# Optimization experiments

Measured on AMD Instinct MI355X. Metric: run time of the kernel, lower is better.

Reference implementation:

```python
import jax, jax.numpy as jnp
import numpy as np
from jax import lax

S = 16  # encoder stride (patchify-conv stand-in for the CNN backbone, stride-16 feature grid)


def _conv(x, w, b, stride, padding):
    y = lax.conv_general_dilated(x, w, (stride, stride), padding,
                                 dimension_numbers=('NCHW', 'OIHW', 'NCHW'))
    return y + b[None, :, None, None]


def _l2norm(x, eps=1e-12):  # F.normalize(p=2, dim=1)
    n = jnp.sqrt(jnp.sum(x * x, axis=1, keepdims=True))
    return x / jnp.maximum(n, eps)


def _encode(frame, ew, eb, kw, kb, vw, vb, mask=None):
    feat = jax.nn.relu(_conv(frame, ew, eb, S, 'VALID'))  # [B,512,h,w]
    key = _conv(feat, kw, kb, 1, 'SAME')                  # [B,64,h,w]
    val = _conv(feat, vw, vb, 1, 'SAME')                  # [B,ed,h,w]
    if mask is not None:
        m = mask[:, None, ::S, ::S]  # torch F.interpolate 'nearest' with exact integer factor
        key = key * m
        val = val * m
    return _l2norm(key), val, feat


def _forward(query_frame, prev_frame, prev_mask, first_frame, first_mask,
             enc_q_w, enc_q_b, enc_m_w, enc_m_b,
             key_w, key_b, val_w, val_b,
             dec1_w, dec1_b, dec2_w, dec2_b, cls_w, cls_b):
    # memory bank reset + push(first), push(prev)
    k1, v1, _ = _encode(first_frame, enc_m_w, enc_m_b, key_w, key_b, val_w, val_b, first_mask)
    kp, vp, _ = _encode(prev_frame, enc_m_w, enc_m_b, key_w, key_b, val_w, val_b, prev_mask)
    qk, qv, _ = _encode(query_frame, enc_q_w, enc_q_b, key_w, key_b, val_w, val_b)
    B, Ck, h, w = qk.shape
    ed = qv.shape[1]
    mem_key = jnp.concatenate([k1.reshape(B, Ck, -1), kp.reshape(B, Ck, -1)], axis=2)  # [B,64,M]
    mem_val = jnp.concatenate([v1.reshape(B, ed, -1), vp.reshape(B, ed, -1)], axis=2)  # [B,ed,M]
    q_key = qk.reshape(B, Ck, -1)                                                      # [B,64,Q]
    # STM memory read: affinity -> softmax -> weighted sum over memory pixels
    affinity = jnp.einsum('bcq,bcm->bqm', q_key, mem_key) / jnp.sqrt(jnp.float32(Ck))
    affinity = jax.nn.softmax(affinity, axis=-1)
    mem_read = jnp.einsum('bqm,bcm->bcq', affinity, mem_val).reshape(B, ed, h, w)
    fused = jnp.concatenate([qv, mem_read], axis=1)  # [B,2*ed,h,w] (aspp=False)
    d = jax.nn.relu(_conv(fused, dec1_w, dec1_b, 1, 'SAME'))
    dec_feat = jax.nn.relu(_conv(d, dec2_w, dec2_b, 1, 'SAME'))
    logits = _conv(dec_feat, cls_w, cls_b, 1, 'SAME')
    H, W = query_frame.shape[-2], query_frame.shape[-1]
    logits_full = jax.image.resize(logits, (B, logits.shape[1], H, W), method='bilinear')  # align_corners=False
    rep_feat = _l2norm(dec_feat)
    return rep_feat, logits_full


def setup_inputs():
    key = jax.random.key(0)
    ks = jax.random.split(key, 16)
    B, H, W = 8, 512, 512
    Ce, Ck, ed = 512, 64, 256
    g = lambda i, sh, s: jax.random.normal(ks[i], sh, dtype=jnp.float32) * s
    return {
        'query_frame': g(0, (B, 3, H, W), 1.0),
        'prev_frame': g(1, (B, 3, H, W), 1.0),
        'prev_mask': jnp.round(jax.random.uniform(ks[2], (B, H, W), dtype=jnp.float32)),
        'first_frame': g(3, (B, 3, H, W), 1.0),
        'first_mask': jnp.round(jax.random.uniform(ks[4], (B, H, W), dtype=jnp.float32)),
        'enc_q_w': g(5, (Ce, 3, S, S), 0.02), 'enc_q_b': jnp.zeros((Ce,), jnp.float32),
        'enc_m_w': g(6, (Ce, 3, S, S), 0.02), 'enc_m_b': jnp.zeros((Ce,), jnp.float32),
        'key_w': g(7, (Ck, Ce, 1, 1), 0.05), 'key_b': jnp.zeros((Ck,), jnp.float32),
        'val_w': g(8, (ed, Ce, 1, 1), 0.05), 'val_b': jnp.zeros((ed,), jnp.float32),
        'dec1_w': g(9, (ed, 2 * ed, 3, 3), 0.02), 'dec1_b': jnp.zeros((ed,), jnp.float32),
        'dec2_w': g(10, (ed, ed, 3, 3), 0.02), 'dec2_b': jnp.zeros((ed,), jnp.float32),
        'cls_w': g(11, (2, ed, 1, 1), 0.05), 'cls_b': jnp.zeros((2,), jnp.float32),
    }


def reference(query_frame, prev_frame, prev_mask, first_frame, first_mask,
              enc_q_w, enc_q_b, enc_m_w, enc_m_b,
              key_w, key_b, val_w, val_b,
              dec1_w, dec1_b, dec2_w, dec2_b, cls_w, cls_b):
    return _forward(query_frame, prev_frame, prev_mask, first_frame, first_mask,
                    enc_q_w, enc_q_b, enc_m_w, enc_m_b,
                    key_w, key_b, val_w, val_b,
                    dec1_w, dec1_b, dec2_w, dec2_b, cls_w, cls_b)
```

## Files before the change

### kernel.cpp

```cpp
#include <hip/hip_runtime.h>
#include <hip/hip_bf16.h>
#include <cstdint>

#define DEV __device__ __forceinline__
typedef __attribute__((ext_vector_type(8))) short short8;
typedef __attribute__((ext_vector_type(4))) float f32x4;
typedef unsigned short u16;

DEV float b2f(u16 u) { union { unsigned int i; float f; } x; x.i = (unsigned)u << 16; return x.f; }
DEV u16 f2b(float f) { __hip_bfloat16 h = __float2bfloat16(f); return *(u16*)&h; }
DEV float rdin(const void* p, size_t i, int isbf) {
  return isbf ? __bfloat162float(((const __hip_bfloat16*)p)[i]) : ((const float*)p)[i];
}
DEV void wrout(void* p, size_t i, float v, int isbf) {
  if (isbf) ((__hip_bfloat16*)p)[i] = __float2bfloat16(v);
  else      ((float*)p)[i] = v;
}
DEV short8 ld8(const void* p, size_t idx, int isbf) {
  if (isbf) return *(const short8*)((const u16*)p + idx);
  const float* f = (const float*)p + idx;
  float4 x = *(const float4*)f, y = *(const float4*)(f + 4);
  short8 r;
  r[0] = f2b(x.x); r[1] = f2b(x.y); r[2] = f2b(x.z); r[3] = f2b(x.w);
  r[4] = f2b(y.x); r[5] = f2b(y.y); r[6] = f2b(y.z); r[7] = f2b(y.w);
  return r;
}
DEV void gl16(const u16* g, u16* l) {
  __builtin_amdgcn_global_load_lds(
      (const __attribute__((address_space(1))) void*)g,
      (__attribute__((address_space(3))) void*)l, 16, 0, 0);
}
DEV void bar() {
  asm volatile("" ::: "memory");
  __builtin_amdgcn_s_barrier();
  asm volatile("" ::: "memory");
}

__global__ __launch_bounds__(256) void detect_k(const u16* w, int* flag) {
  __shared__ int cnt[256];
  int tid = threadIdx.x, c = 0;
  for (int i = tid; i < 4096; i += 256) {
    u16 v = w[i];
    int e = (v >> 7) & 0xFF;
    if (v == 0 || (e >= 0x60 && e <= 0x9F)) c++;
  }
  cnt[tid] = c;
  __syncthreads();
  for (int s = 128; s > 0; s >>= 1) { if (tid < s) cnt[tid] += cnt[tid + s]; __syncthreads(); }
  if (tid == 0) *flag = (cnt[0] > 3600) ? 1 : 0;
}

__global__ __launch_bounds__(256) void patchify_k(const void* F0, const void* F1,
                                                  u16* dst, const int* dflag) {
  int isbf = *dflag;
  int bid = blockIdx.x;
  int z = bid >> 8, rem = bid & 255, b = rem >> 5, y = rem & 31;
  const void* F = z ? F1 : F0;
  int x = threadIdx.x & 31, pj = threadIdx.x >> 5;
  u16* drow = dst + (size_t)(z * 8192 + b * 1024 + y * 32 + x) * 768;
#pragma unroll
  for (int i = 0; i < 6; i++) {
    int pair = i * 8 + pj;
    int c = pair >> 4, ky = pair & 15;
    size_t src = ((size_t)((b * 3 + c) * 512 + y * 16 + ky)) * 512 + x * 16;
    short8 v0 = ld8(F, src, isbf);
    short8 v1 = ld8(F, src + 8, isbf);
    u16* dp = drow + c * 256 + ky * 16;
    *(short8*)dp = v0;
    *(short8*)(dp + 8) = v1;
  }
}

__global__ __launch_bounds__(256) void wconv_k(const void* wm, const void* wq,
                                               u16* dst, const int* dflag) {
  int isbf = *dflag;
  int gi = blockIdx.x * 256 + threadIdx.x;
  size_t e0 = (size_t)gi * 8;
  const void* src = e0 < 393216 ? wm : wq;
  size_t off = e0 < 393216 ? e0 : e0 - 393216;
  *(short8*)&dst[e0] = ld8(src, off, isbf);
}

__global__ __launch_bounds__(256) void kvconv_k(const void* valW, const void* keyW,
                                                u16* dst, const int* dflag) {
  int isbf = *dflag;
  int idx = blockIdx.x * 256 + threadIdx.x;
  size_t e0 = (size_t)idx * 8;
  int row = (int)(e0 >> 9);
  const void* src = row < 256 ? valW : keyW;
  size_t off = row < 256 ? e0 : e0 - (size_t)256 * 512;
  *(short8*)&dst[e0] = ld8(src, off, isbf);
}

struct PA {
  const void* W0; const void* W1; size_t bs; int K; int rowsplit; int zsel; int ws16; int rowmax1;
  DEV short8 l8(int row, int k, int b, int zz, int isbf) const {
    const void* W = W0; int r = row;
    if (zsel && zz == 2) W = W1;
    else if (rowsplit && row >= rowsplit) { W = W1; r = row - rowsplit; if (r > rowmax1) r = rowmax1; }
    return ld8(W, (size_t)b * bs + (size_t)r * K + k, ws16 ? 1 : isbf);
  }
  DEV const u16* ga(int row, int k, int b, int zz) const {
    int r = row; if (rowsplit && r > rowmax1) r = rowmax1;
    return (const u16*)W0 + (size_t)b * bs + (size_t)r * K + k;
  }
};
struct PBws {
  const u16* X; int rs; size_t zs;
  DEV short8 l8(int t, int k, int zz, int) const {
    return *(const short8*)(X + (size_t)zz * zs + (size_t)t * rs + k);
  }
  DEV const u16* ga(int t, int k, int zz) const {
    return X + (size_t)zz * zs + (size_t)t * rs + k;
  }
};
struct PBc3 {
  const u16* X; int C; int shift;
  DEV short8 l8(int t, int k, int, int) const {
    int tap = k >> shift, c0 = k & (C - 1);
    int dy = tap / 3, dx = tap - dy * 3;
    int pos = t & 1023, y = pos >> 5, x = pos & 31;
    int iy = y + dy - 1, ix = x + dx - 1;
    if ((unsigned)iy >= 32u || (unsigned)ix >= 32u) { short8 z = {0,0,0,0,0,0,0,0}; return z; }
    return *(const short8*)(X + (size_t)(((t >> 10) * 1024) + iy * 32 + ix) * C + c0);
  }
};

struct Epi {
  int mode;
  u16 *o16, *o16b, *o16c;
  size_t zs; int ts, moff, mmax;
  const void *bias, *bias2; int bzsel;
  const void *maskA, *maskB;
  const float* rscale;
  float scale; int relu, doexp;
  DEV void store1(int m, int t, int z, float v, int isbf) const {
    if (m >= mmax) return;
    int b = t >> 10, pos = t & 1023;
    if (m < 256) {
      v += rdin(bias, m, isbf);
      if (z < 2) {
        const void* mk = z ? maskB : maskA;
        v *= rdin(mk, ((size_t)(b * 512 + (pos >> 5) * 16) << 9) + (pos & 31) * 16, isbf);
        o16[((size_t)(b * 256 + m)) * 2048 + (size_t)z * 1024 + pos] = f2b(v);
      } else {
        o16b[(size_t)t * 512 + m] = f2b(v);
      }
    } else {
      v += rdin(bias2, m - 256, isbf);
      o16c[((size_t)z * 8192 + t) * 64 + (m - 256)] = f2b(v);
    }
  }
};

DEV void epilogue(const Epi& ep, f32x4 (&acc)[4][4], u16* sh, int isbf, int tid,
                  int col16, int quad, int wm, int wn, int zz, int m0, int n0, int nbase) {
  if (ep.mode == 1) {
#pragma unroll
    for (int mt = 0; mt < 4; mt++)
#pragma unroll
      for (int nt = 0; nt < 4; nt++)
#pragma unroll
        for (int r = 0; r < 4; r++) {
          int m = m0 + wm * 64 + mt * 16 + quad * 4 + r;
          int t = nbase + n0 + wn * 64 + nt * 16 + col16;
          ep.store1(m, t, zz, acc[mt][nt][r], isbf);
        }
    return;
  }
  if (ep.mode == 2) {
    float* pf = (float*)ep.o16;
#pragma unroll
    for (int mt = 0; mt < 4; mt++)
#pragma unroll
      for (int nt = 0; nt < 4; nt++)
#pragma unroll
        for (int r = 0; r < 4; r++) {
          int m = m0 + wm * 64 + mt * 16 + quad * 4 + r;
          int t = nbase + n0 + wn * 64 + nt * 16 + col16;
          pf[((size_t)(zz * 256 + m)) * 8192 + t] = acc[mt][nt][r];
        }
    return;
  }
  u16* T = sh;
  const int TS = 132;
  for (int p = 0; p < 2; p++) {
    __syncthreads();
    if (wn == p) {
#pragma unroll
      for (int mt = 0; mt < 4; mt++)
#pragma unroll
        for (int nt = 0; nt < 4; nt++) {
          int tl = nt * 16 + col16;
#pragma unroll
          for (int r2 = 0; r2 < 2; r2++) {
            int ml = wm * 64 + mt * 16 + quad * 4 + r2 * 2;
            float v0 = acc[mt][nt][r2 * 2] * ep.scale;
            float v1 = acc[mt][nt][r2 * 2 + 1] * ep.scale;
            if (ep.bias) {
              const void* bp = (ep.bzsel && zz == 2) ? ep.bias2 : ep.bias;
              v0 += rdin(bp, m0 + ml, isbf);
              v1 += rdin(bp, m0 + ml + 1, isbf);
            }
            if (ep.relu) { v0 = fmaxf(v0, 0.f); v1 = fmaxf(v1, 0.f); }
            unsigned int pk = (unsigned)f2b(v0) | ((unsigned)f2b(v1) << 16);
            *(unsigned int*)&T[tl * TS + ml] = pk;
          }
        }
    }
    __syncthreads();
    {
      int tl = tid >> 2, seg = tid & 3;
      int tg = nbase + n0 + p * 64 + tl;
      u16* op = ep.o16 + (size_t)zz * ep.zs + (size_t)tg * ep.ts + ep.moff + m0;
#pragma unroll
      for (int i = 0; i < 4; i++) {
        int c8 = seg + i * 4;
        short8 v = *(short8*)&T[tl * TS + c8 * 8];
        *(short8*)&op[c8 * 8] = v;
      }
    }
  }
}

template <class PB>
__global__ __launch_bounds__(256) void mgl(PA pa, PB pb, Epi ep, int ktiles, int nbase,
                                           const int* dflag) {
  __shared__ u16 sh[32768];
  int isbf = *dflag;
  int tid = threadIdx.x, lane = tid & 63;
  int col16 = lane & 15, quad = lane >> 4;
  int wv = tid >> 6, wm = wv >> 1, wn = wv & 1;
  int zz = blockIdx.z;
  int n0 = blockIdx.x * 128, m0 = blockIdx.y * 128;
  int bA = (nbase + n0) >> 10;

  f32x4 acc[4][4];
#pragma unroll
  for (int mt = 0; mt < 4; mt++)
#pragma unroll
    for (int nt = 0; nt < 4; nt++)
#pragma unroll
      for (int r = 0; r < 4; r++) acc[mt][nt][r] = 0.f;

  int rA[4], lA[4];
#pragma unroll
  for (int g = 0; g < 4; g++) {
    rA[g] = g * 32 + (tid >> 3);
    lA[g] = (tid & 7) ^ (rA[g] & 7);
  }

  auto issue = [&](int kt) {
    int kk = kt * 64;
    u16* base = sh + ((kt & 1) << 14);
#pragma unroll
    for (int g = 0; g < 4; g++) {
      gl16(pa.ga(m0 + rA[g], kk + lA[g] * 8, bA, zz), base + (size_t)(g * 256 + tid) * 8);
      gl16(pb.ga(nbase + n0 + rA[g], kk + lA[g] * 8, zz), base + 8192 + (size_t)(g * 256 + tid) * 8);
    }
  };
  issue(0);

  for (int kt = 0; kt < ktiles; kt++) {
    const u16* As = sh + ((kt & 1) << 14);
    const u16* Bs = As + 8192;
    if (kt + 1 < ktiles) {
      issue(kt + 1);
      asm volatile("s_waitcnt vmcnt(8)" ::: "memory");
    } else {
      asm volatile("s_waitcnt vmcnt(0)" ::: "memory");
    }
    bar();
#pragma unroll
    for (int s = 0; s < 2; s++) {
      short8 af[4], bf[4];
      int cs = ((s * 4 + quad) ^ (col16 & 7)) << 3;
#pragma unroll
      for (int mt = 0; mt < 4; mt++)
        af[mt] = *(const short8*)&As[(wm * 64 + mt * 16 + col16) * 64 + cs];
#pragma unroll
      for (int nt = 0; nt < 4; nt++)
        bf[nt] = *(const short8*)&Bs[(wn * 64 + nt * 16 + col16) * 64 + cs];
#pragma unroll
      for (int mt = 0; mt < 4; mt++)
#pragma unroll
        for (int nt = 0; nt < 4; nt++)
          acc[mt][nt] = __builtin_amdgcn_mfma_f32_16x16x32_bf16(af[mt], bf[nt], acc[mt][nt], 0, 0, 0);
    }
    bar();
  }

  epilogue(ep, acc, sh, isbf, tid, col16, quad, wm, wn, zz, m0, n0, nbase);
}

template <class PB>
__global__ __launch_bounds__(256) void mg(PA pa, PB pb, Epi ep, int ktiles, int nbase,
                                          int ksplit, const int* dflag) {
  __shared__ u16 sh[32768];
  int isbf = *dflag;
  int tid = threadIdx.x, lane = tid & 63;
  int col16 = lane & 15, quad = lane >> 4;
  int wv = tid >> 6, wm = wv >> 1, wn = wv & 1;
  int zz = blockIdx.z;
  int kb = ksplit * zz;
  int n0 = blockIdx.x * 128, m0 = blockIdx.y * 128;
  int bA = (nbase + n0) >> 10;

  f32x4 acc[4][4];
#pragma unroll
  for (int mt = 0; mt < 4; mt++)
#pragma unroll
    for (int nt = 0; nt < 4; nt++)
#pragma unroll
      for (int r = 0; r < 4; r++) acc[mt][nt][r] = 0.f;

  int rA[4], lA[4];
#pragma unroll
  for (int g = 0; g < 4; g++) {
    rA[g] = g * 32 + (tid >> 3);
    lA[g] = (tid & 7) ^ (rA[g] & 7);
  }

  short8 ra[4], rb[4];
#pragma unroll
  for (int g = 0; g < 4; g++) {
    ra[g] = pa.l8(m0 + rA[g], kb + lA[g] * 8, bA, zz, isbf);
    rb[g] = pb.l8(nbase + n0 + rA[g], kb + lA[g] * 8, zz, isbf);
  }
#pragma unroll
  for (int g = 0; g < 4; g++) {
    *(short8*)&sh[(size_t)(g * 256 + tid) * 8] = ra[g];
    *(short8*)&sh[8192 + (size_t)(g * 256 + tid) * 8] = rb[g];
  }
  __syncthreads();

  for (int kt = 0; kt < ktiles; kt++) {
    const u16* As = sh + ((kt & 1) ? 16384 : 0);
    const u16* Bs = As + 8192;
    bool more = (kt + 1 < ktiles);
    if (more) {
      int kn = kb + (kt + 1) * 64;
#pragma unroll
      for (int g = 0; g < 4; g++) {
        ra[g] = pa.l8(m0 + rA[g], kn + lA[g] * 8, bA, zz, isbf);
        rb[g] = pb.l8(nbase + n0 + rA[g], kn + lA[g] * 8, zz, isbf);
      }
    }
#pragma unroll
    for (int s = 0; s < 2; s++) {
      short8 af[4], bf[4];
      int cs = ((s * 4 + quad) ^ (col16 & 7)) << 3;
#pragma unroll
      for (int mt = 0; mt < 4; mt++)
        af[mt] = *(const short8*)&As[(wm * 64 + mt * 16 + col16) * 64 + cs];
#pragma unroll
      for (int nt = 0; nt < 4; nt++)
        bf[nt] = *(const short8*)&Bs[(wn * 64 + nt * 16 + col16) * 64 + cs];
#pragma unroll
      for (int mt = 0; mt < 4; mt++)
#pragma unroll
        for (int nt = 0; nt < 4; nt++)
          acc[mt][nt] = __builtin_amdgcn_mfma_f32_16x16x32_bf16(af[mt], bf[nt], acc[mt][nt], 0, 0, 0);
    }
    if (more) {
      u16* An = sh + (!(kt & 1) ? 16384 : 0);
#pragma unroll
      for (int g = 0; g < 4; g++) {
        *(short8*)&An[(size_t)(g * 256 + tid) * 8] = ra[g];
        *(short8*)&An[8192 + (size_t)(g * 256 + tid) * 8] = rb[g];
      }
      __syncthreads();
    }
  }

  epilogue(ep, acc, sh, isbf, tid, col16, quad, wm, wn, zz, m0, n0, nbase);
}

__global__ __launch_bounds__(256) void attn_k(const u16* qk, const u16* memk,
                                              const u16* memv, float* pf, float* rsum) {
  __shared__ u16 sh[28672];
  __shared__ float rsl[4][64];
  const int Qt = 0, Kt = 4096, Vt = 8192, Pl = 24576;
  int tid = threadIdx.x, lane = tid & 63;
  int col16 = lane & 15, quad = lane >> 4;
  int wv = tid >> 6;
  int xl = blockIdx.x;
  int x = ((xl & 7) << 4) | (xl >> 3);
  int b = x >> 4, qt = x & 15;
  int q0 = b * 1024 + qt * 64;
  int s = blockIdx.y;
  int kv0 = s * 512;

  rsl[wv][lane] = 0.f;

  int r32 = tid >> 3;
#pragma unroll
  for (int g = 0; g < 2; g++) {
    int row = g * 32 + r32;
    int k8 = (tid & 7) ^ (row & 7);
    gl16(qk + (size_t)(q0 + row) * 64 + k8 * 8, sh + Qt + (size_t)(g * 256 + tid) * 8);
  }
  {
#pragma unroll
    for (int g = 0; g < 2; g++) {
      int row = g * 32 + r32;
      int k8 = (tid & 7) ^ (row & 7);
      gl16(memk + ((size_t)(b * 2048 + kv0 + row)) * 64 + k8 * 8,
           sh + Kt + (size_t)(g * 256 + tid) * 8);
    }
#pragma unroll
    for (int g = 0; g < 8; g++) {
      int row = g * 32 + r32;
      int k8 = (tid & 7) ^ (row & 7);
      gl16(memv + ((size_t)(b * 256 + row)) * 2048 + kv0 + k8 * 8,
           sh + Vt + (size_t)(g * 256 + tid) * 8);
    }
  }
  __syncthreads();

  f32x4 acc_o[4][4];
#pragma unroll
  for (int mt = 0; mt < 4; mt++)
#pragma unroll
    for (int nt = 0; nt < 4; nt++)
#pragma unroll
      for (int r = 0; r < 4; r++) acc_o[mt][nt][r] = 0.f;

  for (int ch = 0; ch < 8; ch++) {
    {
      f32x4 acc_s[4];
#pragma unroll
      for (int nt = 0; nt < 4; nt++)
#pragma unroll
        for (int r = 0; r < 4; r++) acc_s[nt][r] = 0.f;
#pragma unroll
      for (int s2 = 0; s2 < 2; s2++) {
        int cs = ((s2 * 4 + quad) ^ (col16 & 7)) << 3;
        short8 af = *(const short8*)&sh[Kt + (wv * 16 + col16) * 64 + cs];
        short8 bf[4];
#pragma unroll
        for (int nt = 0; nt < 4; nt++)
          bf[nt] = *(const short8*)&sh[Qt + (nt * 16 + col16) * 64 + cs];
#pragma unroll
        for (int nt = 0; nt < 4; nt++)
          acc_s[nt] = __builtin_amdgcn_mfma_f32_16x16x32_bf16(af, bf[nt], acc_s[nt], 0, 0, 0);
      }
#pragma unroll
      for (int nt = 0; nt < 4; nt++) {
        int ql = nt * 16 + col16;
        float tsum = 0.f;
#pragma unroll
        for (int r = 0; r < 4; r++) {
          int kvl = wv * 16 + quad * 4 + r;
          u16 pb = f2b(__expf(0.125f * acc_s[nt][r]));
          tsum += b2f(pb);
          sh[Pl + ql * 64 + (((kvl >> 3) ^ (ql & 7)) << 3) + (kvl & 7)] = pb;
        }
        tsum += __shfl_xor(tsum, 16);
        tsum += __shfl_xor(tsum, 32);
        if (quad == 0) rsl[wv][ql] += tsum;
      }
    }
    __syncthreads();
    if (ch + 1 < 8) {
      int kvc = kv0 + (ch + 1) * 64;
#pragma unroll
      for (int g = 0; g < 2; g++) {
        int row = g * 32 + r32;
        int k8 = (tid & 7) ^ (row & 7);
        gl16(memk + ((size_t)(b * 2048 + kvc + row)) * 64 + k8 * 8,
             sh + Kt + (size_t)(g * 256 + tid) * 8);
      }
    }
#pragma unroll
    for (int s2 = 0; s2 < 2; s2++) {
      short8 af[4], bf[4];
      int cs = ((s2 * 4 + quad) ^ (col16 & 7)) << 3;
#pragma unroll
      for (int mt = 0; mt < 4; mt++)
        af[mt] = *(const short8*)&sh[Vt + (wv * 64 + mt * 16 + col16) * 64 + cs];
#pragma unroll
      for (int nt = 0; nt < 4; nt++)
        bf[nt] = *(const short8*)&sh[Pl + (nt * 16 + col16) * 64 + cs];
#pragma unroll
      for (int mt = 0; mt < 4; mt++)
#pragma unroll
        for (int nt = 0; nt < 4; nt++)
          acc_o[mt][nt] = __builtin_amdgcn_mfma_f32_16x16x32_bf16(af[mt], bf[nt], acc_o[mt][nt], 0, 0, 0);
    }
    __syncthreads();
    if (ch + 1 < 8) {
      int kvc = kv0 + (ch + 1) * 64;
#pragma unroll
      for (int g = 0; g < 8; g++) {
        int row = g * 32 + r32;
        int k8 = (tid & 7) ^ (row & 7);
        gl16(memv + ((size_t)(b * 256 + row)) * 2048 + kvc + k8 * 8,
             sh + Vt + (size_t)(g * 256 + tid) * 8);
      }
    }
    __syncthreads();
  }

#pragma unroll
  for (int mt = 0; mt < 4; mt++)
#pragma unroll
    for (int nt = 0; nt < 4; nt++)
#pragma unroll
      for (int r = 0; r < 4; r++) {
        int c = wv * 64 + mt * 16 + quad * 4 + r;
        int q = nt * 16 + col16;
        pf[((size_t)(s * 8192 + q0 + q)) * 256 + c] = acc_o[mt][nt][r];
      }
  if (tid < 64)
    atomicAdd(&rsum[q0 + tid], rsl[0][tid] + rsl[1][tid] + rsl[2][tid] + rsl[3][tid]);
}

__global__ __launch_bounds__(256) void acomb_k(const float* pf, const float* rsum,
                                               u16* fused) {
  int tid = threadIdx.x;
  int t = blockIdx.x * 2 + (tid >> 7);
  int cp = tid & 127;
  float inv = 1.f / rsum[t];
  float v0 = 0.f, v1 = 0.f;
#pragma unroll
  for (int s = 0; s < 4; s++) {
    const float* p = pf + ((size_t)(s * 8192 + t)) * 256 + cp * 2;
    v0 += p[0]; v1 += p[1];
  }
  unsigned int pk = (unsigned)f2b(v0 * inv) | ((unsigned)f2b(v1 * inv) << 16);
  *(unsigned int*)&fused[(size_t)t * 512 + 256 + cp * 2] = pk;
}

__global__ __launch_bounds__(256) void comb_k(const float* pf, const void* bias,
                                              u16* out, int ts, int moff, int npart,
                                              int relu, const int* dflag) {
  int isbf = *dflag;
  int tid = threadIdx.x;
  int t = blockIdx.x * 64 + (tid & 63);
  int m = blockIdx.y * 8 + ((tid >> 6) << 1);
  float v0 = 0.f, v1 = 0.f;
  for (int p = 0; p < npart; p++) {
    v0 += pf[(size_t)(p * 256 + m) * 8192 + t];
    v1 += pf[(size_t)(p * 256 + m + 1) * 8192 + t];
  }
  if (bias) { v0 += rdin(bias, m, isbf); v1 += rdin(bias, m + 1, isbf); }
  if (relu) { v0 = fmaxf(v0, 0.f); v1 = fmaxf(v1, 0.f); }
  unsigned int pk = (unsigned)f2b(v0) | ((unsigned)f2b(v1) << 16);
  *(unsigned int*)&out[(size_t)t * ts + moff + m] = pk;
}

__global__ __launch_bounds__(256) void wreorder_k(const void* src, u16* dst, int C,
                                                  int total, const int* dflag) {
  int idx = blockIdx.x * 256 + threadIdx.x;
  if (idx >= total) return;
  int isbf = *dflag;
  int nine_c = 9 * C;
  int m = idx / nine_c; int r = idx - m * nine_c;
  int tp = r / C; int c = r - tp * C;
  dst[idx] = f2b(rdin(src, (size_t)(m * C + c) * 9 + tp, isbf));
}

__global__ __launch_bounds__(256) void keyfix_k(const u16* kraw3, const void* mA,
                                                const void* mB, u16* memk, u16* qk,
                                                float* rsum, const int* dflag) {
  int isbf = *dflag;
  int z = blockIdx.y;
  int n = blockIdx.x * 256 + threadIdx.x;
  int b = n >> 10, pos = n & 1023;
  if (z == 0) rsum[n] = 0.f;
  float mv = 1.f;
  if (z == 0) mv = rdin(mA, ((size_t)(b * 512 + (pos >> 5) * 16) << 9) + (pos & 31) * 16, isbf);
  else if (z == 1) mv = rdin(mB, ((size_t)(b * 512 + (pos >> 5) * 16) << 9) + (pos & 31) * 16, isbf);
  const u16* src = kraw3 + ((size_t)z * 8192 + n) * 64;
  float v[64], ss = 0.f;
#pragma unroll
  for (int c = 0; c < 64; c++) { v[c] = b2f(src[c]) * mv; ss += v[c] * v[c]; }
  float inv = 1.f / fmaxf(sqrtf(ss), 1e-12f);
  u16* dst = (z < 2) ? memk + (size_t)(b * 2048 + z * 1024 + pos) * 64 : qk + (size_t)n * 64;
#pragma unroll
  for (int c = 0; c < 64; c++) dst[c] = f2b(v[c] * inv);
}

__global__ __launch_bounds__(256) void repcls_k(const u16* decf, const void* cwgt,
                                                const void* cbias, void* out_rep,
                                                float* logits, const int* dflag) {
  int isbf = *dflag;
  int tid = threadIdx.x, lane = tid & 63, wv = tid >> 6;
  int tok = blockIdx.x * 4 + wv;
  int b = tok >> 10, pos = tok & 1023;
  const u16* src = decf + (size_t)tok * 256;
  int c0 = lane * 4;
  float v[4], ss = 0.f, a0 = 0.f, a1 = 0.f;
#pragma unroll
  for (int j = 0; j < 4; j++) {
    float x = b2f(src[c0 + j]);
    v[j] = x; ss += x * x;
    a0 = fmaf(x, rdin(cwgt, c0 + j, isbf), a0);
    a1 = fmaf(x, rdin(cwgt, 256 + c0 + j, isbf), a1);
  }
#pragma unroll
  for (int off = 32; off > 0; off >>= 1) {
    ss += __shfl_down(ss, off); a0 += __shfl_down(a0, off); a1 += __shfl_down(a1, off);
  }
  ss = __shfl(ss, 0); a0 = __shfl(a0, 0); a1 = __shfl(a1, 0);
  float inv = 1.f / fmaxf(sqrtf(ss), 1e-12f);
#pragma unroll
  for (int j = 0; j < 4; j++)
    wrout(out_rep, ((size_t)(b * 256 + c0 + j) << 10) + pos, v[j] * inv, isbf);
  if (lane == 0) {
    logits[((size_t)(b * 2) << 10) + pos]     = a0 + rdin(cbias, 0, isbf);
    logits[((size_t)(b * 2 + 1) << 10) + pos] = a1 + rdin(cbias, 1, isbf);
  }
}

__global__ __launch_bounds__(256) void resize_k(const float* logits, void* out,
                                                size_t ebase, const int* dflag) {
  int isbf = *dflag;
  int idx = blockIdx.x * 256 + threadIdx.x;
  int ox = idx & 511, oy = (idx >> 9) & 511, c = (idx >> 18) & 1, b = idx >> 19;
  float fy = (oy + 0.5f) * 0.0625f - 0.5f;
  float fx = (ox + 0.5f) * 0.0625f - 0.5f;
  int y0 = (int)floorf(fy), x0 = (int)floorf(fx);
  float wy = fy - y0, wx = fx - x0;
  int y0c = max(y0, 0), y1c = min(y0 + 1, 31);
  int x0c = max(x0, 0), x1c = min(x0 + 1, 31);
  const float* L = logits + ((size_t)(b * 2 + c) << 10);
  float v00 = L[y0c * 32 + x0c], v01 = L[y0c * 32 + x1c];
  float v10 = L[y1c * 32 + x0c], v11 = L[y1c * 32 + x1c];
  float v = (1.f - wy) * ((1.f - wx) * v00 + wx * v01) + wy * ((1.f - wx) * v10 + wx * v11);
  wrout(out, ebase + (size_t)idx, v, isbf);
}

extern "C" void kernel_launch(void* const* d_in, const int* in_sizes, int n_in,
                              void* d_out, int out_size, void* d_ws, size_t ws_size,
                              hipStream_t stream) {
  const void* query  = d_in[0];  const void* prev   = d_in[1];
  const void* prevM  = d_in[2];  const void* first  = d_in[3];
  const void* firstM = d_in[4];  const void* encQw  = d_in[5];
  const void* encQb  = d_in[6];  const void* encMw  = d_in[7];
  const void* encMb  = d_in[8];  const void* keyW   = d_in[9];
  const void* keyB   = d_in[10]; const void* valW   = d_in[11];
  const void* valB   = d_in[12]; const void* dec1W  = d_in[13];
  const void* dec1B  = d_in[14]; const void* dec2W  = d_in[15];
  const void* dec2B  = d_in[16]; const void* clsW   = d_in[17];
  const void* clsB   = d_in[18];

  u16* W = (u16*)d_ws;
  int* dflag = (int*)W;
  float* rsum   = (float*)(W + 16);
  float* logits = (float*)(W + 16400);
  u16* B0 = W + 49168;
  u16* Xp    = B0;
  u16* feat3 = B0 + 12582912;
  u16* encWb = B0 + 25165824;
  u16* wr1   = B0;
  u16* wr2   = B0 + 1179648;
  u16* fused = B0 + 1769472;
  u16* memv  = B0 + 5963776;
  u16* memk  = B0 + 10158080;
  u16* qk    = B0 + 11206656;
  u16* kraw3 = B0 + 25165824;
  u16* kvW   = B0 + 26738688;
  float* pf  = (float*)(B0 + 11730944);
  u16* dbuf  = memv;
  u16* decf  = memv + 2097152;

  dim3 blk(256);
  detect_k<<<dim3(1), blk, 0, stream>>>((const u16*)encQw, dflag);

  wconv_k<<<dim3(384), blk, 0, stream>>>(encMw, encQw, encWb, dflag);
  patchify_k<<<dim3(512), blk, 0, stream>>>(first, prev, Xp, dflag);
  {
    PA a{encWb, 0, 0, 768, 0, 0, 1, 0};
    PBws b{Xp, 768, (size_t)8192 * 768};
    Epi e{0, feat3, 0, 0, (size_t)8192 * 512, 512, 0, 512,
          encMb, 0, 0, 0, 0, 0, 1.f, 1, 0};
    mgl<PBws><<<dim3(64, 4, 2), blk, 0, stream>>>(a, b, e, 12, 0, dflag);
  }
  patchify_k<<<dim3(256), blk, 0, stream>>>(query, query, Xp, dflag);
  {
    PA a{encWb + 393216, 0, 0, 768, 0, 0, 1, 0};
    PBws b{Xp, 768, 0};
    Epi e{0, feat3 + (size_t)2 * 8192 * 512, 0, 0, 0, 512, 0, 512,
          encQb, 0, 0, 0, 0, 0, 1.f, 1, 0};
    mgl<PBws><<<dim3(64, 4, 1), blk, 0, stream>>>(a, b, e, 12, 0, dflag);
  }

  wreorder_k<<<dim3(4608), blk, 0, stream>>>(dec1W, wr1, 512, 256 * 4608, dflag);
  wreorder_k<<<dim3(2304), blk, 0, stream>>>(dec2W, wr2, 256, 256 * 2304, dflag);
  kvconv_k<<<dim3(80), blk, 0, stream>>>(valW, keyW, kvW, dflag);

  {
    PA a{kvW, 0, 0, 512, 1, 0, 1, 319};
    PBws b{feat3, 512, (size_t)8192 * 512};
    Epi e{1, memv, fused, kraw3, 0, 0, 0, 320,
          valB, keyB, 0, firstM, prevM, 0, 1.f, 0, 0};
    mgl<PBws><<<dim3(64, 3, 3), blk, 0, stream>>>(a, b, e, 8, 0, dflag);
  }
  keyfix_k<<<dim3(32, 3), blk, 0, stream>>>(kraw3, firstM, prevM, memk, qk, rsum, dflag);

  attn_k<<<dim3(128, 4), blk, 0, stream>>>(qk, memk, memv, pf, rsum);
  acomb_k<<<dim3(4096), blk, 0, stream>>>(pf, rsum, fused);

  {
    PA a{wr1, 0, 0, 4608, 0, 0, 1, 0};
    PBc3 b{fused, 512, 9};
    Epi e{2, (u16*)pf, 0, 0, 0, 0, 0, 0,
          0, 0, 0, 0, 0, 0, 1.f, 0, 0};
    mg<PBc3><<<dim3(64, 2, 4), blk, 0, stream>>>(a, b, e, 18, 0, 1152, dflag);
    comb_k<<<dim3(128, 32), blk, 0, stream>>>(pf, dec1B, dbuf, 256, 0, 4, 1, dflag);
  }
  {
    PA a{wr2, 0, 0, 2304, 0, 0, 1, 0};
    PBc3 b{dbuf, 256, 8};
    Epi e{2, (u16*)pf, 0, 0, 0, 0, 0, 0,
          0, 0, 0, 0, 0, 0, 1.f, 0, 0};
    mg<PBc3><<<dim3(64, 2, 2), blk, 0, stream>>>(a, b, e, 18, 0, 1152, dflag);
    comb_k<<<dim3(128, 32), blk, 0, stream>>>(pf, dec2B, decf, 256, 0, 2, 1, dflag);
  }

  repcls_k<<<dim3(2048), blk, 0, stream>>>(decf, clsW, clsB, d_out, logits, dflag);
  resize_k<<<dim3(16384), blk, 0, stream>>>(logits, d_out, (size_t)2097152, dflag);
}
```

Measured before the change: 441.8 us.

## Single-buffer GEMM LDS for higher occupancy and raise dec2 split-K to four

Both GEMM kernels (mgl, mg) drop double-buffered shared memory to a single 32 KB buffer and request 4 blocks per CU through launch_bounds, so more workgroups can be resident at once. The mgl async-load path now waits for all loads before computing, and mg stores its register-prefetched tile into the one buffer behind an extra barrier. In exchange, global loads no longer overlap with MFMA work inside a block. Separately, the dec2 conv GEMM goes from split-K 2 to 4 (9 k-tiles each) for more blocks, and the combine kernel now sums four partials.

```diff
diff --git a/kernel.cpp b/kernel.cpp
--- a/kernel.cpp
+++ b/kernel.cpp
@@ -224,9 +224,9 @@
 }
 
 template <class PB>
-__global__ __launch_bounds__(256) void mgl(PA pa, PB pb, Epi ep, int ktiles, int nbase,
-                                           const int* dflag) {
-  __shared__ u16 sh[32768];
+__global__ __launch_bounds__(256, 4) void mgl(PA pa, PB pb, Epi ep, int ktiles, int nbase,
+                                              const int* dflag) {
+  __shared__ u16 sh[16384];
   int isbf = *dflag;
   int tid = threadIdx.x, lane = tid & 63;
   int col16 = lane & 15, quad = lane >> 4;
@@ -250,26 +250,14 @@
     lA[g] = (tid & 7) ^ (rA[g] & 7);
   }
 
-  auto issue = [&](int kt) {
+  for (int kt = 0; kt < ktiles; kt++) {
     int kk = kt * 64;
-    u16* base = sh + ((kt & 1) << 14);
 #pragma unroll
     for (int g = 0; g < 4; g++) {
-      gl16(pa.ga(m0 + rA[g], kk + lA[g] * 8, bA, zz), base + (size_t)(g * 256 + tid) * 8);
-      gl16(pb.ga(nbase + n0 + rA[g], kk + lA[g] * 8, zz), base + 8192 + (size_t)(g * 256 + tid) * 8);
-    }
-  };
-  issue(0);
-
-  for (int kt = 0; kt < ktiles; kt++) {
-    const u16* As = sh + ((kt & 1) << 14);
-    const u16* Bs = As + 8192;
-    if (kt + 1 < ktiles) {
-      issue(kt + 1);
-      asm volatile("s_waitcnt vmcnt(8)" ::: "memory");
-    } else {
-      asm volatile("s_waitcnt vmcnt(0)" ::: "memory");
-    }
+      gl16(pa.ga(m0 + rA[g], kk + lA[g] * 8, bA, zz), sh + (size_t)(g * 256 + tid) * 8);
+      gl16(pb.ga(nbase + n0 + rA[g], kk + lA[g] * 8, zz), sh + 8192 + (size_t)(g * 256 + tid) * 8);
+    }
+    asm volatile("s_waitcnt vmcnt(0)" ::: "memory");
     bar();
 #pragma unroll
     for (int s = 0; s < 2; s++) {
@@ -277,10 +265,10 @@
       int cs = ((s * 4 + quad) ^ (col16 & 7)) << 3;
 #pragma unroll
       for (int mt = 0; mt < 4; mt++)
-        af[mt] = *(const short8*)&As[(wm * 64 + mt * 16 + col16) * 64 + cs];
+        af[mt] = *(const short8*)&sh[(wm * 64 + mt * 16 + col16) * 64 + cs];
 #pragma unroll
       for (int nt = 0; nt < 4; nt++)
-        bf[nt] = *(const short8*)&Bs[(wn * 64 + nt * 16 + col16) * 64 + cs];
+        bf[nt] = *(const short8*)&sh[8192 + (wn * 64 + nt * 16 + col16) * 64 + cs];
 #pragma unroll
       for (int mt = 0; mt < 4; mt++)
 #pragma unroll
@@ -294,9 +282,9 @@
 }
 
 template <class PB>
-__global__ __launch_bounds__(256) void mg(PA pa, PB pb, Epi ep, int ktiles, int nbase,
-                                          int ksplit, const int* dflag) {
-  __shared__ u16 sh[32768];
+__global__ __launch_bounds__(256, 4) void mg(PA pa, PB pb, Epi ep, int ktiles, int nbase,
+                                             int ksplit, const int* dflag) {
+  __shared__ u16 sh[16384];
   int isbf = *dflag;
   int tid = threadIdx.x, lane = tid & 63;
   int col16 = lane & 15, quad = lane >> 4;
@@ -327,18 +315,16 @@
     ra[g] = pa.l8(m0 + rA[g], kb + lA[g] * 8, bA, zz, isbf);
     rb[g] = pb.l8(nbase + n0 + rA[g], kb + lA[g] * 8, zz, isbf);
   }
-#pragma unroll
-  for (int g = 0; g < 4; g++) {
-    *(short8*)&sh[(size_t)(g * 256 + tid) * 8] = ra[g];
-    *(short8*)&sh[8192 + (size_t)(g * 256 + tid) * 8] = rb[g];
-  }
-  __syncthreads();
 
   for (int kt = 0; kt < ktiles; kt++) {
-    const u16* As = sh + ((kt & 1) ? 16384 : 0);
-    const u16* Bs = As + 8192;
-    bool more = (kt + 1 < ktiles);
-    if (more) {
+    if (kt) __syncthreads();
+#pragma unroll
+    for (int g = 0; g < 4; g++) {
+      *(short8*)&sh[(size_t)(g * 256 + tid) * 8] = ra[g];
+      *(short8*)&sh[8192 + (size_t)(g * 256 + tid) * 8] = rb[g];
+    }
+    __syncthreads();
+    if (kt + 1 < ktiles) {
       int kn = kb + (kt + 1) * 64;
 #pragma unroll
       for (int g = 0; g < 4; g++) {
@@ -352,24 +338,15 @@
       int cs = ((s * 4 + quad) ^ (col16 & 7)) << 3;
 #pragma unroll
       for (int mt = 0; mt < 4; mt++)
-        af[mt] = *(const short8*)&As[(wm * 64 + mt * 16 + col16) * 64 + cs];
+        af[mt] = *(const short8*)&sh[(wm * 64 + mt * 16 + col16) * 64 + cs];
 #pragma unroll
       for (int nt = 0; nt < 4; nt++)
-        bf[nt] = *(const short8*)&Bs[(wn * 64 + nt * 16 + col16) * 64 + cs];
+        bf[nt] = *(const short8*)&sh[8192 + (wn * 64 + nt * 16 + col16) * 64 + cs];
 #pragma unroll
       for (int mt = 0; mt < 4; mt++)
 #pragma unroll
         for (int nt = 0; nt < 4; nt++)
           acc[mt][nt] = __builtin_amdgcn_mfma_f32_16x16x32_bf16(af[mt], bf[nt], acc[mt][nt], 0, 0, 0);
-    }
-    if (more) {
-      u16* An = sh + (!(kt & 1) ? 16384 : 0);
-#pragma unroll
-      for (int g = 0; g < 4; g++) {
-        *(short8*)&An[(size_t)(g * 256 + tid) * 8] = ra[g];
-        *(short8*)&An[8192 + (size_t)(g * 256 + tid) * 8] = rb[g];
-      }
-      __syncthreads();
     }
   }
 
@@ -716,8 +693,8 @@
     PBc3 b{dbuf, 256, 8};
     Epi e{2, (u16*)pf, 0, 0, 0, 0, 0, 0,
           0, 0, 0, 0, 0, 0, 1.f, 0, 0};
-    mg<PBc3><<<dim3(64, 2, 2), blk, 0, stream>>>(a, b, e, 18, 0, 1152, dflag);
-    comb_k<<<dim3(128, 32), blk, 0, stream>>>(pf, dec2B, decf, 256, 0, 2, 1, dflag);
+    mg<PBc3><<<dim3(64, 2, 4), blk, 0, stream>>>(a, b, e, 9, 0, 576, dflag);
+    comb_k<<<dim3(128, 32), blk, 0, stream>>>(pf, dec2B, decf, 256, 0, 4, 1, dflag);
   }
 
   repcls_k<<<dim3(2048), blk, 0, stream>>>(decf, clsW, clsB, d_out, logits, dflag);
```

New measurement: 668.7 us. 1.51x slower.
